# Kernel optimization log

Hardware: AMD Instinct MI355X
Metric: run time of the kernel (lower is better)

Reference implementation:

```python
import jax, jax.numpy as jnp
import numpy as np

N = 65536      # detector nodes (hits)
P = 128        # particles
DIM = 3
N_NEAREST = 5
EPS = 1e-8
BIG = 999.0


def setup_inputs() -> dict:
    key = jax.random.key(0)
    ks = jax.random.split(key, 9)
    x = jax.random.normal(ks[0], (N, DIM), jnp.float32)
    q = jax.random.uniform(ks[1], (N,), jnp.float32)
    is_cond_point = (jax.random.uniform(ks[2], (N,)) < 0.2).astype(jnp.float32)
    beta = jax.random.uniform(ks[3], (N,), jnp.float32)
    node_class = jax.random.randint(ks[4], (N,), 0, 6).astype(jnp.float32)
    max_x = jax.random.normal(ks[5], (P, DIM), jnp.float32)
    max_q = jax.random.uniform(ks[6], (P,), jnp.float32) + 0.5
    particle_class = jax.random.randint(ks[7], (P,), 0, 6).astype(jnp.float32)
    parent_target = jax.random.randint(ks[8], (N,), 0, P, dtype=jnp.int32)
    particle_idx = jnp.arange(P, dtype=jnp.int32)
    return dict(x=x, q=q, is_cond_point=is_cond_point, beta=beta,
                node_class=node_class, max_x=max_x, max_q=max_q,
                particle_class=particle_class, parent_target=parent_target,
                particle_idx=particle_idx)


def _rms_stats(dx, dxq, belongs, q_mailbox, cond_dist):
    # dx/dxq/belongs/cond_dist: [C, N] mailboxes (C receivers, each sees all N nodes)
    Np = belongs.sum(axis=1)                                   # [C]
    rms = jnp.sqrt(jnp.sum((dx * belongs) ** 2, axis=1) / Np)
    sum_q = jnp.sum(q_mailbox)  # NOTE: original sums the ENTIRE mailbox (quirk kept)
    rmsq = jnp.sqrt(jnp.sum(dxq ** 2, axis=1) / (Np * sum_q))
    cond = jnp.where(cond_dist < EPS, BIG, cond_dist)
    nn = -jax.lax.top_k(-cond, N_NEAREST)[0]  # 5 smallest, ascending == sort+slice
    return rms, rmsq, Np, nn


def reference(x, q, is_cond_point, beta, node_class, max_x, max_q, particle_class,
              parent_target, particle_idx):
    # --- update_all node_to_particle (message_dist -> compute_rms) ---
    dx = jnp.linalg.norm(x[None, :, :] - max_x[:, None, :], axis=-1)          # [P,N]
    belongs = (parent_target[None, :] == particle_idx[:, None]).astype(dx.dtype)
    dxq = dx * q[None, :] * max_q[:, None]
    cond = dx * is_cond_point[None, :]
    q_mb = jnp.broadcast_to(q[None, :], dx.shape)
    rms, rmsq, Np, nn = _rms_stats(dx, dxq, belongs, q_mb, cond)

    # --- update_all nodes->global (dst lacks 'max x'/'max q'/'particle idx') ---
    dxg = jnp.linalg.norm(x, axis=-1)[None, :]                                # [1,N]
    dxqg = dxg * q[None, :]
    belongs_g = jnp.ones_like(dxg)
    cond_g = dxg * is_cond_point[None, :]
    rms_g, rmsq_g, Ng, nn_g = _rms_stats(dxg, dxqg, belongs_g, q[None, :], cond_g)

    # --- update_all particles->global: Davies-Bouldin over [P,P] pairs ---
    DS = rms[:, None] + rms[None, :]                                          # Si+Sj
    M2 = jnp.sum((max_x[:, None, :] - max_x[None, :, :]) ** 2, axis=-1)       # ||xi-xj||^2
    R = jnp.where(M2 > 0, DS / jnp.where(M2 > 0, M2, 1.0), 0.0)               # nan/inf->0
    db = jnp.mean(jnp.max(R, axis=1))                                         # (1/P) sum_i max_j

    # --- update_all particle_to_node: node inherits its parent particle's N ---
    N_node = jnp.einsum('pn,p->n', belongs, Np)                               # [N]

    # --- apply_edges particle_to_node: ||max_x_p - x_n|| and membership ---
    dist_edge = dx            # [P,N], identical math to edges' 'dist x'
    belongs_edge = belongs    # [P,N]; beta/class edge feats are pure broadcasts

    return (rms, rmsq, Np, nn, rms_g, rmsq_g, Ng, nn_g, db,
            N_node, dist_edge, belongs_edge)
```

## Files before the change

### kernel.cpp

```cpp
#include <hip/hip_runtime.h>

#define NN 65536
#define PP 128
#define EPSV 1e-8f
#define BIGV 999.0f
#define PGRP 8

typedef float f32x4 __attribute__((ext_vector_type(4)));

#define O_RMS   0
#define O_RMSQ  128
#define O_NP    256
#define O_NN    384
#define O_RMSG  1024
#define O_RMSQG 1025
#define O_NG    1026
#define O_NNG   1027
#define O_DB    1032
#define O_NNODE 1033
#define O_DIST  66569
#define O_BEL   (66569 + 8388608)

#define W_BS   0
#define W_PP   512
#define W_CNT  41472
#define W_X4   41536
#define W_CL4  303680

__device__ inline float wred(float v) {
#pragma unroll
  for (int o = 32; o > 0; o >>= 1) v += __shfl_down(v, o, 64);
  return v;
}

__device__ inline void t5ins(float t[5], float v) {
  if (v < t[4]) {
    t[4] = v;
#pragma unroll
    for (int k = 4; k > 0; --k)
      if (t[k] < t[k - 1]) { float tm = t[k]; t[k] = t[k - 1]; t[k - 1] = tm; }
  }
}

__device__ inline void merge5(const float* a, const float* b, float* o) {
  int i = 0, j = 0;
#pragma unroll
  for (int k = 0; k < 5; ++k) {
    float av = a[i], bv = b[j];
    if (av <= bv) { o[k] = av; ++i; } else { o[k] = bv; ++j; }
  }
}

__global__ __launch_bounds__(256) void k1_nodes(const float* __restrict__ x,
                                                const float* __restrict__ q,
                                                const float* __restrict__ ic,
                                                const int* __restrict__ par,
                                                float* __restrict__ ws) {
  __shared__ float ps[640];
  __shared__ float wsum[4][8];
  __shared__ int lcnt;
  int tid = threadIdx.x, b = blockIdx.x;
  for (int i = tid; i < 640; i += 256) ps[i] = 0.f;
  if (tid == 0) lcnt = 0;
  __syncthreads();
  float A = 0.f, B0 = 0.f, B1 = 0.f, B2 = 0.f, Cq = 0.f, Sq = 0.f, Sxx = 0.f;
  float4* xp4 = (float4*)(ws + W_X4);
  float4* cl4 = (float4*)(ws + W_CL4);
  int base = b * 1024;
#pragma unroll
  for (int it = 0; it < 4; ++it) {
    int n = base + it * 256 + tid;
    float x0 = x[3 * n], x1 = x[3 * n + 1], x2 = x[3 * n + 2];
    float qn = q[n], icn = ic[n];
    int pa = par[n];
    float xx = fmaf(x0, x0, fmaf(x1, x1, x2 * x2));
    float q2 = qn * qn;
    A = fmaf(q2, xx, A); B0 = fmaf(q2, x0, B0);
    B1 = fmaf(q2, x1, B1); B2 = fmaf(q2, x2, B2);
    Cq += q2; Sq += qn; Sxx += xx;
    xp4[n] = make_float4(x0, x1, x2, __int_as_float(pa));
    atomicAdd(&ps[pa], x0);
    atomicAdd(&ps[128 + pa], x1);
    atomicAdd(&ps[256 + pa], x2);
    atomicAdd(&ps[384 + pa], xx);
    atomicAdd(&ps[512 + pa], 1.0f);
    if (icn != 0.0f) {
      int loc = atomicAdd(&lcnt, 1);
      cl4[base + loc] = make_float4(x0, x1, x2, icn);
    }
  }
  A = wred(A); B0 = wred(B0); B1 = wred(B1); B2 = wred(B2);
  Cq = wred(Cq); Sq = wred(Sq); Sxx = wred(Sxx);
  int w = tid >> 6, lane = tid & 63;
  if (lane == 0) {
    wsum[w][0] = A; wsum[w][1] = B0; wsum[w][2] = B1; wsum[w][3] = B2;
    wsum[w][4] = Cq; wsum[w][5] = Sq; wsum[w][6] = Sxx;
  }
  __syncthreads();
  if (tid < 7)
    ws[W_BS + b * 8 + tid] = wsum[0][tid] + wsum[1][tid] + wsum[2][tid] + wsum[3][tid];
  if (tid == 0) ((int*)ws)[W_CNT + b] = lcnt;
  for (int i = tid; i < 640; i += 256) ws[W_PP + b * 640 + i] = ps[i];
}

__global__ __launch_bounds__(256) void k2_edges(const float* __restrict__ mx,
                                                const float* __restrict__ ws,
                                                float* __restrict__ out) {
  __shared__ float smx[PGRP * 3];
  __shared__ float snp[128];
  int tid = threadIdx.x;
  int by = blockIdx.y;
  int p0 = by * PGRP;
  if (tid < PGRP * 3) smx[tid] = mx[p0 * 3 + tid];
  if (by == 0 && tid < 128) {
    float s = 0.f;
    for (int b = 0; b < 64; ++b) s += ws[W_PP + b * 640 + 512 + tid];
    snp[tid] = s;
  }
  __syncthreads();
  const float4* xp4 = (const float4*)(ws + W_X4);
  int v = blockIdx.x * 256 + tid;
  if (v < 16383) {
    int n0 = 3 + 4 * v;
    float4 e0 = xp4[n0], e1 = xp4[n0 + 1], e2 = xp4[n0 + 2], e3 = xp4[n0 + 3];
    int pa0 = __float_as_int(e0.w), pa1 = __float_as_int(e1.w);
    int pa2 = __float_as_int(e2.w), pa3 = __float_as_int(e3.w);
    if (by == 0) {
      f32x4 nn4 = {snp[pa0], snp[pa1], snp[pa2], snp[pa3]};
      __builtin_nontemporal_store(nn4, (f32x4*)(out + O_NNODE + n0));
    }
#pragma unroll
    for (int pi = 0; pi < PGRP; ++pi) {
      int p = p0 + pi;
      float m0 = smx[3 * pi], m1 = smx[3 * pi + 1], m2 = smx[3 * pi + 2];
      f32x4 d, bl;
      float d0, d1, d2;
      d0 = e0.x - m0; d1 = e0.y - m1; d2 = e0.z - m2;
      d.x = sqrtf(fmaf(d0, d0, fmaf(d1, d1, d2 * d2)));
      d0 = e1.x - m0; d1 = e1.y - m1; d2 = e1.z - m2;
      d.y = sqrtf(fmaf(d0, d0, fmaf(d1, d1, d2 * d2)));
      d0 = e2.x - m0; d1 = e2.y - m1; d2 = e2.z - m2;
      d.z = sqrtf(fmaf(d0, d0, fmaf(d1, d1, d2 * d2)));
      d0 = e3.x - m0; d1 = e3.y - m1; d2 = e3.z - m2;
      d.w = sqrtf(fmaf(d0, d0, fmaf(d1, d1, d2 * d2)));
      bl.x = (pa0 == p) ? 1.f : 0.f; bl.y = (pa1 == p) ? 1.f : 0.f;
      bl.z = (pa2 == p) ? 1.f : 0.f; bl.w = (pa3 == p) ? 1.f : 0.f;
      size_t ro = (size_t)p * NN + n0;
      __builtin_nontemporal_store(d,  (f32x4*)(out + O_DIST + ro));
      __builtin_nontemporal_store(bl, (f32x4*)(out + O_BEL + ro));
    }
  } else if (v == 16383) {
    float4 es[4] = {xp4[0], xp4[1], xp4[2], xp4[65535]};
    int ns[4] = {0, 1, 2, 65535};
#pragma unroll
    for (int k = 0; k < 4; ++k) {
      int pa = __float_as_int(es[k].w);
      if (by == 0)
        __builtin_nontemporal_store(snp[pa], out + O_NNODE + ns[k]);
#pragma unroll
      for (int pi = 0; pi < PGRP; ++pi) {
        int p = p0 + pi;
        float m0 = smx[3 * pi], m1 = smx[3 * pi + 1], m2 = smx[3 * pi + 2];
        float d0 = es[k].x - m0, d1 = es[k].y - m1, d2 = es[k].z - m2;
        float dd = sqrtf(fmaf(d0, d0, fmaf(d1, d1, d2 * d2)));
        size_t ro = (size_t)p * NN + ns[k];
        __builtin_nontemporal_store(dd, out + O_DIST + ro);
        __builtin_nontemporal_store((pa == p) ? 1.f : 0.f, out + O_BEL + ro);
      }
    }
  }
}

__global__ __launch_bounds__(256) void k3_top5fin(const float* __restrict__ mx,
                                                  const float* __restrict__ mq,
                                                  const float* __restrict__ ws,
                                                  float* __restrict__ out) {
  int tid = threadIdx.x;
  int r = blockIdx.x;
  if (r < 129) {
    __shared__ int cnts[64];
    __shared__ float sl[1280];
    float m0 = 0.f, m1 = 0.f, m2 = 0.f;
    if (r < 128) { m0 = mx[3 * r]; m1 = mx[3 * r + 1]; m2 = mx[3 * r + 2]; }
    if (tid < 64) cnts[tid] = ((const int*)ws)[W_CNT + tid];
    __syncthreads();
    const float4* cl4 = (const float4*)(ws + W_CL4);
    float t[5] = {BIGV, BIGV, BIGV, BIGV, BIGV};
    for (int seg = 0; seg < 64; ++seg) {
      int c = cnts[seg];
      for (int i = tid; i < c; i += 256) {
        float4 e = cl4[seg * 1024 + i];
        float d0 = e.x - m0, d1 = e.y - m1, d2 = e.z - m2;
        float dd = sqrtf(fmaf(d0, d0, fmaf(d1, d1, d2 * d2)));
        float vv = dd * e.w;
        vv = (vv < EPSV) ? BIGV : vv;
        t5ins(t, vv);
      }
    }
#pragma unroll
    for (int k = 0; k < 5; ++k) sl[tid * 5 + k] = t[k];
    __syncthreads();
    for (int s = 128; s >= 1; s >>= 1) {
      if (tid < s) {
        float a[5], b[5], o[5];
#pragma unroll
        for (int k = 0; k < 5; ++k) { a[k] = sl[tid * 5 + k]; b[k] = sl[(tid + s) * 5 + k]; }
        merge5(a, b, o);
#pragma unroll
        for (int k = 0; k < 5; ++k) sl[tid * 5 + k] = o[k];
      }
      __syncthreads();
    }
    if (tid == 0) {
      float* dst = (r < 128) ? (out + O_NN + 5 * r) : (out + O_NNG);
#pragma unroll
      for (int k = 0; k < 5; ++k) dst[k] = sl[k];
    }
  } else {
    __shared__ float gs[8];
    __shared__ float srms[128], smx2[384], wsum2[2];
    if (tid < 64) {
      float a0 = ws[W_BS + tid * 8 + 0], a1 = ws[W_BS + tid * 8 + 1];
      float a2 = ws[W_BS + tid * 8 + 2], a3 = ws[W_BS + tid * 8 + 3];
      float a4 = ws[W_BS + tid * 8 + 4], a5 = ws[W_BS + tid * 8 + 5];
      float a6 = ws[W_BS + tid * 8 + 6];
      a0 = wred(a0); a1 = wred(a1); a2 = wred(a2); a3 = wred(a3);
      a4 = wred(a4); a5 = wred(a5); a6 = wred(a6);
      if (tid == 0) {
        gs[0] = a0; gs[1] = a1; gs[2] = a2; gs[3] = a3;
        gs[4] = a4; gs[5] = a5; gs[6] = a6;
      }
    }
    __syncthreads();
    int p = tid;
    float rms = 0.f, m0 = 0.f, m1 = 0.f, m2 = 0.f;
    if (p < 128) {
      float A = gs[0], B0 = gs[1], B1 = gs[2], B2 = gs[3];
      float Cq = gs[4], Sq = gs[5];
      float sx0 = 0.f, sx1 = 0.f, sx2 = 0.f, sxx = 0.f, cnt = 0.f;
      for (int b = 0; b < 64; ++b) {
        const float* pp = ws + W_PP + b * 640;
        sx0 += pp[p]; sx1 += pp[128 + p]; sx2 += pp[256 + p];
        sxx += pp[384 + p]; cnt += pp[512 + p];
      }
      m0 = mx[3 * p]; m1 = mx[3 * p + 1]; m2 = mx[3 * p + 2];
      float mqv = mq[p];
      float mm = fmaf(m0, m0, fmaf(m1, m1, m2 * m2));
      float s1 = fmaxf(sxx - 2.f * (m0 * sx0 + m1 * sx1 + m2 * sx2) + mm * cnt, 0.f);
      rms = sqrtf(s1 / cnt);
      float s2 = fmaxf(A - 2.f * (m0 * B0 + m1 * B1 + m2 * B2) + mm * Cq, 0.f);
      float rmsq = sqrtf(mqv * mqv * s2 / (cnt * ((float)PP * Sq)));
      out[O_RMS + p] = rms; out[O_RMSQ + p] = rmsq; out[O_NP + p] = cnt;
      if (p == 0) {
        out[O_RMSG]  = sqrtf(gs[6] / (float)NN);
        out[O_RMSQG] = sqrtf(gs[0] / ((float)NN * Sq));
        out[O_NG]    = (float)NN;
      }
      srms[p] = rms;
      smx2[3 * p] = m0; smx2[3 * p + 1] = m1; smx2[3 * p + 2] = m2;
    }
    __syncthreads();
    if (p < 128) {
      float mr = 0.f;
      for (int j = 0; j < PP; ++j) {
        float d0 = m0 - smx2[3 * j], d1 = m1 - smx2[3 * j + 1], d2 = m2 - smx2[3 * j + 2];
        float M2 = fmaf(d0, d0, fmaf(d1, d1, d2 * d2));
        float rr = (M2 > 0.f) ? (rms + srms[j]) / M2 : 0.f;
        mr = fmaxf(mr, rr);
      }
      float sred = wred(mr);
      if ((p & 63) == 0) wsum2[p >> 6] = sred;
    }
    __syncthreads();
    if (tid == 0) out[O_DB] = (wsum2[0] + wsum2[1]) * (1.0f / 128.0f);
  }
}

extern "C" void kernel_launch(void* const* d_in, const int* in_sizes, int n_in,
                              void* d_out, int out_size, void* d_ws, size_t ws_size,
                              hipStream_t stream) {
  const float* x  = (const float*)d_in[0];
  const float* q  = (const float*)d_in[1];
  const float* ic = (const float*)d_in[2];
  const float* mx = (const float*)d_in[5];
  const float* mq = (const float*)d_in[6];
  const int*   par = (const int*)d_in[8];
  float* out = (float*)d_out;
  float* ws = (float*)d_ws;

  hipLaunchKernelGGL(k1_nodes,   dim3(64),      dim3(256), 0, stream, x, q, ic, par, ws);
  hipLaunchKernelGGL(k2_edges,   dim3(64, 16),  dim3(256), 0, stream, mx, ws, out);
  hipLaunchKernelGGL(k3_top5fin, dim3(130),     dim3(256), 0, stream, mx, mq, ws, out);
}
```

Measured before the change: 67.40 us.

## Merge node-stats and edge-writing kernels into one launch, moving N_node to finalize

The per-node statistics kernel and the big dist/belongs edge-writing kernel are merged into a single launch. Edge blocks now read x and parent_target directly from the inputs through shared memory instead of waiting on a packed float4 staging buffer, so the two no longer have to run one after the other. The N_node gather, which needs the global per-particle counts, moves into extra blocks of the final kernel. This removes one launch and the dependency barrier plus the staging write and read, at the cost of a more complex shared-memory staging layout and an extra gather of par in the last kernel.

After: 58.36 us. 1.15x faster.

```diff
diff --git a/kernel.cpp b/kernel.cpp
--- a/kernel.cpp
+++ b/kernel.cpp
@@ -4,9 +4,9 @@
 #define PP 128
 #define EPSV 1e-8f
 #define BIGV 999.0f
-#define PGRP 8
 
 typedef float f32x4 __attribute__((ext_vector_type(4)));
+typedef int   i32x4 __attribute__((ext_vector_type(4)));
 
 #define O_RMS   0
 #define O_RMSQ  128
@@ -24,7 +24,6 @@
 #define W_BS   0
 #define W_PP   512
 #define W_CNT  41472
-#define W_X4   41536
 #define W_CL4  303680
 
 __device__ inline float wred(float v) {
@@ -51,135 +50,146 @@
   }
 }
 
-__global__ __launch_bounds__(256) void k1_nodes(const float* __restrict__ x,
-                                                const float* __restrict__ q,
-                                                const float* __restrict__ ic,
-                                                const int* __restrict__ par,
-                                                float* __restrict__ ws) {
-  __shared__ float ps[640];
-  __shared__ float wsum[4][8];
-  __shared__ int lcnt;
-  int tid = threadIdx.x, b = blockIdx.x;
-  for (int i = tid; i < 640; i += 256) ps[i] = 0.f;
-  if (tid == 0) lcnt = 0;
-  __syncthreads();
-  float A = 0.f, B0 = 0.f, B1 = 0.f, B2 = 0.f, Cq = 0.f, Sq = 0.f, Sxx = 0.f;
-  float4* xp4 = (float4*)(ws + W_X4);
-  float4* cl4 = (float4*)(ws + W_CL4);
-  int base = b * 1024;
-#pragma unroll
-  for (int it = 0; it < 4; ++it) {
-    int n = base + it * 256 + tid;
-    float x0 = x[3 * n], x1 = x[3 * n + 1], x2 = x[3 * n + 2];
-    float qn = q[n], icn = ic[n];
-    int pa = par[n];
-    float xx = fmaf(x0, x0, fmaf(x1, x1, x2 * x2));
-    float q2 = qn * qn;
-    A = fmaf(q2, xx, A); B0 = fmaf(q2, x0, B0);
-    B1 = fmaf(q2, x1, B1); B2 = fmaf(q2, x2, B2);
-    Cq += q2; Sq += qn; Sxx += xx;
-    xp4[n] = make_float4(x0, x1, x2, __int_as_float(pa));
-    atomicAdd(&ps[pa], x0);
-    atomicAdd(&ps[128 + pa], x1);
-    atomicAdd(&ps[256 + pa], x2);
-    atomicAdd(&ps[384 + pa], xx);
-    atomicAdd(&ps[512 + pa], 1.0f);
-    if (icn != 0.0f) {
-      int loc = atomicAdd(&lcnt, 1);
-      cl4[base + loc] = make_float4(x0, x1, x2, icn);
-    }
-  }
-  A = wred(A); B0 = wred(B0); B1 = wred(B1); B2 = wred(B2);
-  Cq = wred(Cq); Sq = wred(Sq); Sxx = wred(Sxx);
-  int w = tid >> 6, lane = tid & 63;
-  if (lane == 0) {
-    wsum[w][0] = A; wsum[w][1] = B0; wsum[w][2] = B1; wsum[w][3] = B2;
-    wsum[w][4] = Cq; wsum[w][5] = Sq; wsum[w][6] = Sxx;
-  }
-  __syncthreads();
-  if (tid < 7)
-    ws[W_BS + b * 8 + tid] = wsum[0][tid] + wsum[1][tid] + wsum[2][tid] + wsum[3][tid];
-  if (tid == 0) ((int*)ws)[W_CNT + b] = lcnt;
-  for (int i = tid; i < 640; i += 256) ws[W_PP + b * 640 + i] = ps[i];
-}
-
-__global__ __launch_bounds__(256) void k2_edges(const float* __restrict__ mx,
-                                                const float* __restrict__ ws,
-                                                float* __restrict__ out) {
-  __shared__ float smx[PGRP * 3];
-  __shared__ float snp[128];
-  int tid = threadIdx.x;
-  int by = blockIdx.y;
-  int p0 = by * PGRP;
-  if (tid < PGRP * 3) smx[tid] = mx[p0 * 3 + tid];
-  if (by == 0 && tid < 128) {
-    float s = 0.f;
-    for (int b = 0; b < 64; ++b) s += ws[W_PP + b * 640 + 512 + tid];
-    snp[tid] = s;
-  }
-  __syncthreads();
-  const float4* xp4 = (const float4*)(ws + W_X4);
-  int v = blockIdx.x * 256 + tid;
-  if (v < 16383) {
-    int n0 = 3 + 4 * v;
-    float4 e0 = xp4[n0], e1 = xp4[n0 + 1], e2 = xp4[n0 + 2], e3 = xp4[n0 + 3];
-    int pa0 = __float_as_int(e0.w), pa1 = __float_as_int(e1.w);
-    int pa2 = __float_as_int(e2.w), pa3 = __float_as_int(e3.w);
-    if (by == 0) {
-      f32x4 nn4 = {snp[pa0], snp[pa1], snp[pa2], snp[pa3]};
-      __builtin_nontemporal_store(nn4, (f32x4*)(out + O_NNODE + n0));
-    }
-#pragma unroll
-    for (int pi = 0; pi < PGRP; ++pi) {
-      int p = p0 + pi;
-      float m0 = smx[3 * pi], m1 = smx[3 * pi + 1], m2 = smx[3 * pi + 2];
-      f32x4 d, bl;
-      float d0, d1, d2;
-      d0 = e0.x - m0; d1 = e0.y - m1; d2 = e0.z - m2;
-      d.x = sqrtf(fmaf(d0, d0, fmaf(d1, d1, d2 * d2)));
-      d0 = e1.x - m0; d1 = e1.y - m1; d2 = e1.z - m2;
-      d.y = sqrtf(fmaf(d0, d0, fmaf(d1, d1, d2 * d2)));
-      d0 = e2.x - m0; d1 = e2.y - m1; d2 = e2.z - m2;
-      d.z = sqrtf(fmaf(d0, d0, fmaf(d1, d1, d2 * d2)));
-      d0 = e3.x - m0; d1 = e3.y - m1; d2 = e3.z - m2;
-      d.w = sqrtf(fmaf(d0, d0, fmaf(d1, d1, d2 * d2)));
-      bl.x = (pa0 == p) ? 1.f : 0.f; bl.y = (pa1 == p) ? 1.f : 0.f;
-      bl.z = (pa2 == p) ? 1.f : 0.f; bl.w = (pa3 == p) ? 1.f : 0.f;
-      size_t ro = (size_t)p * NN + n0;
-      __builtin_nontemporal_store(d,  (f32x4*)(out + O_DIST + ro));
-      __builtin_nontemporal_store(bl, (f32x4*)(out + O_BEL + ro));
-    }
-  } else if (v == 16383) {
-    float4 es[4] = {xp4[0], xp4[1], xp4[2], xp4[65535]};
-    int ns[4] = {0, 1, 2, 65535};
-#pragma unroll
-    for (int k = 0; k < 4; ++k) {
-      int pa = __float_as_int(es[k].w);
-      if (by == 0)
-        __builtin_nontemporal_store(snp[pa], out + O_NNODE + ns[k]);
-#pragma unroll
-      for (int pi = 0; pi < PGRP; ++pi) {
+__global__ __launch_bounds__(256) void kA(const float* __restrict__ x,
+                                          const float* __restrict__ q,
+                                          const float* __restrict__ ic,
+                                          const int* __restrict__ par,
+                                          const float* __restrict__ mx,
+                                          float* __restrict__ ws,
+                                          float* __restrict__ out) {
+  __shared__ __align__(16) float sbuf[4132];
+  int tid = threadIdx.x, bx = blockIdx.x;
+  if (bx < 64) {
+    float* ps = sbuf;
+    float* wsum = sbuf + 640;
+    int* lcnt = (int*)(sbuf + 672);
+    int b = bx;
+    for (int i = tid; i < 640; i += 256) ps[i] = 0.f;
+    if (tid == 0) *lcnt = 0;
+    __syncthreads();
+    float A = 0.f, B0 = 0.f, B1 = 0.f, B2 = 0.f, Cq = 0.f, Sq = 0.f, Sxx = 0.f;
+    float4* cl4 = (float4*)(ws + W_CL4);
+    int base = b * 1024;
+#pragma unroll
+    for (int it = 0; it < 4; ++it) {
+      int n = base + it * 256 + tid;
+      float x0 = x[3 * n], x1 = x[3 * n + 1], x2 = x[3 * n + 2];
+      float qn = q[n], icn = ic[n];
+      int pa = par[n];
+      float xx = fmaf(x0, x0, fmaf(x1, x1, x2 * x2));
+      float q2 = qn * qn;
+      A = fmaf(q2, xx, A); B0 = fmaf(q2, x0, B0);
+      B1 = fmaf(q2, x1, B1); B2 = fmaf(q2, x2, B2);
+      Cq += q2; Sq += qn; Sxx += xx;
+      atomicAdd(&ps[pa], x0);
+      atomicAdd(&ps[128 + pa], x1);
+      atomicAdd(&ps[256 + pa], x2);
+      atomicAdd(&ps[384 + pa], xx);
+      atomicAdd(&ps[512 + pa], 1.0f);
+      if (icn != 0.0f) {
+        int loc = atomicAdd(lcnt, 1);
+        cl4[base + loc] = make_float4(x0, x1, x2, icn);
+      }
+    }
+    A = wred(A); B0 = wred(B0); B1 = wred(B1); B2 = wred(B2);
+    Cq = wred(Cq); Sq = wred(Sq); Sxx = wred(Sxx);
+    int w = tid >> 6, lane = tid & 63;
+    if (lane == 0) {
+      wsum[w * 8 + 0] = A; wsum[w * 8 + 1] = B0; wsum[w * 8 + 2] = B1;
+      wsum[w * 8 + 3] = B2; wsum[w * 8 + 4] = Cq; wsum[w * 8 + 5] = Sq;
+      wsum[w * 8 + 6] = Sxx;
+    }
+    __syncthreads();
+    if (tid < 7)
+      ws[W_BS + b * 8 + tid] =
+          wsum[tid] + wsum[8 + tid] + wsum[16 + tid] + wsum[24 + tid];
+    if (tid == 0) ((int*)ws)[W_CNT + b] = *lcnt;
+    for (int i = tid; i < 640; i += 256) ws[W_PP + b * 640 + i] = ps[i];
+  } else {
+    float* sx = sbuf;
+    int* spar = (int*)(sbuf + 3080);
+    float* smx = sbuf + 4108;
+    int e = bx - 64;
+    int ey = e >> 6, ex = e & 63;
+    int p0 = ey * 8;
+    if (tid < 24) smx[tid] = mx[p0 * 3 + tid];
+    for (int i = tid; i < 770; i += 256) {
+      int g4 = 768 * ex + 2 + i;
+      if (g4 < 49152) *(f32x4*)(sx + 4 * i) = ((const f32x4*)x)[g4];
+    }
+    for (int i = tid; i < 257; i += 256) {
+      int g4 = 256 * ex + i;
+      if (g4 < 16384) *(i32x4*)(spar + 4 * i) = ((const i32x4*)par)[g4];
+    }
+    __syncthreads();
+    int v = ex * 256 + tid;
+    if (v < 16383) {
+      int n0 = 3 + 4 * v;
+      int lx = 1 + 12 * tid;
+      float xv[12];
+#pragma unroll
+      for (int j = 0; j < 12; ++j) xv[j] = sx[lx + j];
+      int lp = 3 + 4 * tid;
+      int pa0 = spar[lp], pa1 = spar[lp + 1], pa2 = spar[lp + 2], pa3 = spar[lp + 3];
+#pragma unroll
+      for (int pi = 0; pi < 8; ++pi) {
         int p = p0 + pi;
         float m0 = smx[3 * pi], m1 = smx[3 * pi + 1], m2 = smx[3 * pi + 2];
-        float d0 = es[k].x - m0, d1 = es[k].y - m1, d2 = es[k].z - m2;
-        float dd = sqrtf(fmaf(d0, d0, fmaf(d1, d1, d2 * d2)));
-        size_t ro = (size_t)p * NN + ns[k];
-        __builtin_nontemporal_store(dd, out + O_DIST + ro);
-        __builtin_nontemporal_store((pa == p) ? 1.f : 0.f, out + O_BEL + ro);
+        f32x4 d, bl;
+        float d0, d1, d2;
+        d0 = xv[0] - m0; d1 = xv[1] - m1; d2 = xv[2] - m2;
+        d.x = sqrtf(fmaf(d0, d0, fmaf(d1, d1, d2 * d2)));
+        d0 = xv[3] - m0; d1 = xv[4] - m1; d2 = xv[5] - m2;
+        d.y = sqrtf(fmaf(d0, d0, fmaf(d1, d1, d2 * d2)));
+        d0 = xv[6] - m0; d1 = xv[7] - m1; d2 = xv[8] - m2;
+        d.z = sqrtf(fmaf(d0, d0, fmaf(d1, d1, d2 * d2)));
+        d0 = xv[9] - m0; d1 = xv[10] - m1; d2 = xv[11] - m2;
+        d.w = sqrtf(fmaf(d0, d0, fmaf(d1, d1, d2 * d2)));
+        bl.x = (pa0 == p) ? 1.f : 0.f; bl.y = (pa1 == p) ? 1.f : 0.f;
+        bl.z = (pa2 == p) ? 1.f : 0.f; bl.w = (pa3 == p) ? 1.f : 0.f;
+        size_t ro = (size_t)p * NN + n0;
+        __builtin_nontemporal_store(d,  (f32x4*)(out + O_DIST + ro));
+        __builtin_nontemporal_store(bl, (f32x4*)(out + O_BEL + ro));
+      }
+    } else if (v == 16383) {
+      float xs[4][3];
+      int pas[4];
+      int ns[4] = {0, 1, 2, 65535};
+#pragma unroll
+      for (int k = 0; k < 3; ++k) {
+        xs[k][0] = x[3 * k]; xs[k][1] = x[3 * k + 1]; xs[k][2] = x[3 * k + 2];
+        pas[k] = par[k];
+      }
+      xs[3][0] = sx[3061]; xs[3][1] = sx[3062]; xs[3][2] = sx[3063];
+      pas[3] = spar[1023];
+#pragma unroll
+      for (int k = 0; k < 4; ++k) {
+#pragma unroll
+        for (int pi = 0; pi < 8; ++pi) {
+          int p = p0 + pi;
+          float m0 = smx[3 * pi], m1 = smx[3 * pi + 1], m2 = smx[3 * pi + 2];
+          float d0 = xs[k][0] - m0, d1 = xs[k][1] - m1, d2 = xs[k][2] - m2;
+          float dd = sqrtf(fmaf(d0, d0, fmaf(d1, d1, d2 * d2)));
+          size_t ro = (size_t)p * NN + ns[k];
+          __builtin_nontemporal_store(dd, out + O_DIST + ro);
+          __builtin_nontemporal_store((pas[k] == p) ? 1.f : 0.f, out + O_BEL + ro);
+        }
       }
     }
   }
 }
 
-__global__ __launch_bounds__(256) void k3_top5fin(const float* __restrict__ mx,
-                                                  const float* __restrict__ mq,
-                                                  const float* __restrict__ ws,
-                                                  float* __restrict__ out) {
+__global__ __launch_bounds__(256) void kB(const float* __restrict__ mx,
+                                          const float* __restrict__ mq,
+                                          const float* __restrict__ ws,
+                                          const int* __restrict__ par,
+                                          float* __restrict__ out) {
+  __shared__ __align__(16) float sb[1344];
   int tid = threadIdx.x;
   int r = blockIdx.x;
   if (r < 129) {
-    __shared__ int cnts[64];
-    __shared__ float sl[1280];
+    int* cnts = (int*)sb;
+    float* sl = sb + 64;
     float m0 = 0.f, m1 = 0.f, m2 = 0.f;
     if (r < 128) { m0 = mx[3 * r]; m1 = mx[3 * r + 1]; m2 = mx[3 * r + 2]; }
     if (tid < 64) cnts[tid] = ((const int*)ws)[W_CNT + tid];
@@ -216,9 +226,11 @@
 #pragma unroll
       for (int k = 0; k < 5; ++k) dst[k] = sl[k];
     }
-  } else {
-    __shared__ float gs[8];
-    __shared__ float srms[128], smx2[384], wsum2[2];
+  } else if (r == 129) {
+    float* gs = sb;
+    float* srms = sb + 8;
+    float* smx2 = sb + 136;
+    float* wsum2 = sb + 520;
     if (tid < 64) {
       float a0 = ws[W_BS + tid * 8 + 0], a1 = ws[W_BS + tid * 8 + 1];
       float a2 = ws[W_BS + tid * 8 + 2], a3 = ws[W_BS + tid * 8 + 3];
@@ -273,6 +285,26 @@
     }
     __syncthreads();
     if (tid == 0) out[O_DB] = (wsum2[0] + wsum2[1]) * (1.0f / 128.0f);
+  } else {
+    float* snp = sb;
+    if (tid < 128) {
+      float s = 0.f;
+      for (int b = 0; b < 64; ++b) s += ws[W_PP + b * 640 + 512 + tid];
+      snp[tid] = s;
+    }
+    __syncthreads();
+    int r2 = r - 130;
+    int v = r2 * 256 + tid;
+    if (v < 16383) {
+      int n0 = 3 + 4 * v;
+      f32x4 o = {snp[par[n0]], snp[par[n0 + 1]], snp[par[n0 + 2]], snp[par[n0 + 3]]};
+      __builtin_nontemporal_store(o, (f32x4*)(out + O_NNODE + n0));
+    } else if (v == 16383) {
+      int ns[4] = {0, 1, 2, 65535};
+#pragma unroll
+      for (int k = 0; k < 4; ++k)
+        __builtin_nontemporal_store(snp[par[ns[k]]], out + O_NNODE + ns[k]);
+    }
   }
 }
 
@@ -288,7 +320,6 @@
   float* out = (float*)d_out;
   float* ws = (float*)d_ws;
 
-  hipLaunchKernelGGL(k1_nodes,   dim3(64),      dim3(256), 0, stream, x, q, ic, par, ws);
-  hipLaunchKernelGGL(k2_edges,   dim3(64, 16),  dim3(256), 0, stream, mx, ws, out);
-  hipLaunchKernelGGL(k3_top5fin, dim3(130),     dim3(256), 0, stream, mx, mq, ws, out);
-}
+  hipLaunchKernelGGL(kA, dim3(1088), dim3(256), 0, stream, x, q, ic, par, mx, ws, out);
+  hipLaunchKernelGGL(kB, dim3(194),  dim3(256), 0, stream, mx, mq, ws, par, out);
+}
```
